# Kernel optimization log

Hardware: AMD Instinct MI355X
Metric: run time of the kernel (lower is better)

The kernel has to match this reference:

```python
import jax, jax.numpy as jnp
import numpy as np

EPS = 1e-06
K = 32


def setup_inputs() -> dict:
    key = jax.random.key(0)
    k1, k2, k3, k4, k5 = jax.random.split(key, 5)
    d_model, n_latents = 1024, 16384
    x = jax.random.normal(k1, (2, 2048, d_model), dtype=jnp.float32)
    b_pre = jax.random.normal(k2, (d_model,), dtype=jnp.float32) * 0.02
    W_enc = jax.random.normal(k3, (n_latents, d_model), dtype=jnp.float32) / np.sqrt(d_model)
    b_enc = jax.random.normal(k4, (n_latents,), dtype=jnp.float32) * 0.02
    W_dec = jax.random.normal(k5, (d_model, n_latents), dtype=jnp.float32)
    # mimic normalize_decoder_weights: unit norm along dim=1 (n_latents axis per row)
    W_dec = W_dec / jnp.linalg.norm(W_dec, axis=1, keepdims=True)
    return {"x": x, "b_pre": b_pre, "W_enc": W_enc, "b_enc": b_enc, "W_dec": W_dec}


def reference(x, b_pre, W_enc, b_enc, W_dec):
    B, S, D = x.shape
    # preprocess: center + normalize (torch .std is unbiased, ddof=1)
    mean = jnp.mean(x, axis=-1, keepdims=True)
    norm = jnp.std(x, axis=-1, keepdims=True, ddof=1) + EPS
    xn = ((x - mean) / norm).reshape(-1, D)          # [N, D]
    # encode
    h = (xn - b_pre) @ W_enc.T + b_enc               # [N, n_latents]
    # top-k + relu + scatter into sparse latent
    vals, idx = jax.lax.top_k(h, K)                  # [N, K]
    vals = jax.nn.relu(vals)
    rows = jnp.arange(h.shape[0])[:, None]
    h_sparse = jnp.zeros_like(h).at[rows, idx].set(vals)
    # decode (dense matmul over mostly-zero latents, as in the original)
    recon = h_sparse @ W_dec.T + b_pre               # [N, D]
    # postprocess: denormalize
    recon = recon.reshape(B, S, D) * norm + mean
    return recon
```

## Files before the change

kernel.cpp:

```cpp
#include <hip/hip_runtime.h>
#include <cstdint>
#include <cstddef>

typedef _Float16 half_t;
typedef _Float16 half4_t __attribute__((ext_vector_type(4)));
typedef _Float16 half8_t __attribute__((ext_vector_type(8)));
typedef unsigned short ushort8_t __attribute__((ext_vector_type(8)));
typedef float floatx4 __attribute__((ext_vector_type(4)));

#define NROWS 4096
#define DMODEL 1024
#define NLAT 16384
#define CAND_MAX 256

#define MBYTE (1ull << 20)
static const size_t oW0    = 0;
static const size_t oWdT   = 32 * MBYTE;
static const size_t oMeanD = 64 * MBYTE;
static const size_t oNormD = 64 * MBYTE + (64ull << 10);
static const size_t oCandC = 64 * MBYTE + (128ull << 10);
static const size_t oCandI = 65 * MBYTE;
static const size_t oBatch = 69 * MBYTE;

#define BATCH_ROW_BYTES 34816ull

__device__ __forceinline__ void gload16(const void* g, void* l) {
  __builtin_amdgcn_global_load_lds(
      (const __attribute__((address_space(1))) void*)g,
      (__attribute__((address_space(3))) void*)l, 16, 0, 0);
}

#define WSPLIT_B 2048
#define TRANS_B  4096
__global__ __launch_bounds__(256) void prepro_kernel(
    const float* __restrict__ x, const float* __restrict__ b_pre,
    const float* __restrict__ W_enc, const float* __restrict__ Wd,
    half_t* __restrict__ W0h, half_t* __restrict__ WdT,
    half_t* __restrict__ X0,
    double* __restrict__ meanD, double* __restrict__ normD, int r0) {
  int bid = blockIdx.x, tid = threadIdx.x;
  if (bid < WSPLIT_B) {
    size_t base = (size_t)bid * 2048 + tid;
    for (int it = 0; it < 8; ++it) {
      size_t i = base + (size_t)it * 256;
      float4 v = ((const float4*)W_enc)[i];
      half4_t h0;
      h0[0] = (half_t)(v.x * 1024.0f);
      h0[1] = (half_t)(v.y * 1024.0f);
      h0[2] = (half_t)(v.z * 1024.0f);
      h0[3] = (half_t)(v.w * 1024.0f);
      ((half4_t*)W0h)[i] = h0;
    }
    return;
  }
  if (bid < WSPLIT_B + TRANS_B) {
    __shared__ float tile[64][65];
    int t = bid - WSPLIT_B;
    int c0 = (t & 255) * 64;
    int r0t = (t >> 8) * 64;
    int tc = tid & 63, tg = tid >> 6;
    for (int i = 0; i < 16; ++i) {
      int rr = i * 4 + tg;
      tile[rr][tc] = Wd[(size_t)(r0t + rr) * NLAT + c0 + tc];
    }
    __syncthreads();
    for (int i = 0; i < 16; ++i) {
      int cc = i * 4 + tg;
      WdT[(size_t)(c0 + cc) * DMODEL + r0t + tc] = (half_t)tile[tc][cc];
    }
    return;
  }
  int rl = bid - WSPLIT_B - TRANS_B;
  int rg = r0 + rl;
  const float4* px = (const float4*)(x + (size_t)rg * DMODEL);
  float4 v = px[tid];
  double s  = (double)v.x + (double)v.y + (double)v.z + (double)v.w;
  double sq = (double)v.x * v.x + (double)v.y * v.y +
              (double)v.z * v.z + (double)v.w * v.w;
  for (int off = 32; off; off >>= 1) {
    s += __shfl_down(s, off);
    sq += __shfl_down(sq, off);
  }
  __shared__ double ss[4], ssq[4];
  __shared__ double sMean, sNorm;
  int wv = tid >> 6, ln = tid & 63;
  if (ln == 0) { ss[wv] = s; ssq[wv] = sq; }
  __syncthreads();
  if (tid == 0) {
    double S = ss[0] + ss[1] + ss[2] + ss[3];
    double Q = ssq[0] + ssq[1] + ssq[2] + ssq[3];
    double mean = S / (double)DMODEL;
    double var = (Q - (double)DMODEL * mean * mean) / (double)(DMODEL - 1);
    double nrm = sqrt(var) + 1e-6;
    sMean = mean; sNorm = nrm;
    meanD[rg] = mean; normD[rg] = nrm;
  }
  __syncthreads();
  float mean = (float)sMean, nrm = (float)sNorm;
  const float4* pb = (const float4*)b_pre;
  float4 bp = pb[tid];
  float c[4];
  c[0] = ((v.x - mean) / nrm - bp.x) * 1024.0f;
  c[1] = ((v.y - mean) / nrm - bp.y) * 1024.0f;
  c[2] = ((v.z - mean) / nrm - bp.z) * 1024.0f;
  c[3] = ((v.w - mean) / nrm - bp.w) * 1024.0f;
  half4_t h0;
  for (int i = 0; i < 4; ++i) h0[i] = (half_t)c[i];
  ((half4_t*)(X0 + (size_t)rl * DMODEL))[tid] = h0;
}

struct SmemAB { half_t A[2][256 * 64]; half_t B[2][256 * 64]; };
union SmemU { SmemAB ab; half_t c[256 * 256]; };

__global__ __launch_bounds__(512, 2) void gemm_enc(
    const half_t* __restrict__ X0, const half_t* __restrict__ W0,
    const float* __restrict__ b_enc, half_t* __restrict__ h, int mtiles) {
  __shared__ __align__(16) SmemU smem;
#define AS(b) (smem.ab.A[b])
#define BS(b) (smem.ab.B[b])
  int tid = threadIdx.x;
  int lane = tid & 63, wave = tid >> 6;
  int wm = wave >> 2, wn = wave & 3;

  int bid = blockIdx.x;
  int xcd = bid & 7, q = bid >> 3;
  int bn = xcd * 8 + (q & 7);
  int bm = q >> 3;
  (void)mtiles;

  const char* Ag = (const char*)(X0 + (size_t)bm * 256 * DMODEL);
  const char* Bg = (const char*)(W0 + (size_t)bn * 256 * DMODEL);

  int srcSwz = ((lane & 7) ^ (lane >> 3)) << 4;
  int rowBase = wave * 8 + (lane >> 3);
  int ldsWOff = wave * 1024;

#define STG_A(b, kt, pr) { int colB = ((kt) & 15) * 128 + srcSwz;             \
    gload16(Ag + (size_t)((pr) * 64 + rowBase) * 2048 + colB,                 \
            (char*)AS(b) + (pr) * 8192 + ldsWOff);                            \
    gload16(Ag + (size_t)(((pr) + 2) * 64 + rowBase) * 2048 + colB,           \
            (char*)AS(b) + ((pr) + 2) * 8192 + ldsWOff); }
#define STG_B(b, kt, pr) { int colB = ((kt) & 15) * 128 + srcSwz;             \
    gload16(Bg + (size_t)((pr) * 64 + rowBase) * 2048 + colB,                 \
            (char*)BS(b) + (pr) * 8192 + ldsWOff);                            \
    gload16(Bg + (size_t)(((pr) + 2) * 64 + rowBase) * 2048 + colB,           \
            (char*)BS(b) + ((pr) + 2) * 8192 + ldsWOff); }

  floatx4 acc[8][4] = {};

  STG_B(0, 0, 0); STG_B(0, 0, 1); STG_A(0, 0, 0); STG_A(0, 0, 1);
  STG_B(1, 1, 0); STG_B(1, 1, 1); STG_A(1, 1, 0);
  asm volatile("s_waitcnt vmcnt(6)" ::: "memory");
  __builtin_amdgcn_sched_barrier(0);
  __builtin_amdgcn_s_barrier();

  int laneQ = (lane & 15) * 128 + (lane >> 4) * 16;
  int sxor = (lane & 7) << 4;
  int aRow = wm * 128 * 128;
  int bRow = wn * 64 * 128;

  half8_t bfr[2][4], afA[4], afB[4];
  const char *Ab, *Bb;

#define LD_B(kk) _Pragma("unroll") for (int t = 0; t < 4; ++t)                \
    bfr[kk][t] = *(const half8_t*)(Bb + ((bRow + t * 2048 +                   \
                                          (kk) * 64 + laneQ) ^ sxor));
#define LD_AF(DST, mh, kk) _Pragma("unroll") for (int t = 0; t < 4; ++t)      \
    DST[t] = *(const half8_t*)(Ab + ((aRow + ((mh) * 4 + t) * 2048 +          \
                                      (kk) * 64 + laneQ) ^ sxor));
#define MM(mb, FR, kk) __builtin_amdgcn_s_setprio(1);                         \
    _Pragma("unroll") for (int mi = 0; mi < 4; ++mi)                          \
    _Pragma("unroll") for (int ni = 0; ni < 4; ++ni)                          \
      acc[(mb) + mi][ni] = __builtin_amdgcn_mfma_f32_16x16x32_f16(            \
          FR[mi], bfr[kk][ni], acc[(mb) + mi][ni], 0, 0, 0);                  \
    __builtin_amdgcn_s_setprio(0);
#define BAR() __builtin_amdgcn_s_barrier()
#define LGKM(n) { asm volatile("s_waitcnt lgkmcnt(" #n ")" ::: "memory");     \
    __builtin_amdgcn_sched_barrier(0); }
#define VM6() { asm volatile("s_waitcnt vmcnt(6)" ::: "memory");              \
    __builtin_amdgcn_sched_barrier(0); }
#define VM0() { asm volatile("s_waitcnt vmcnt(0)" ::: "memory");              \
    __builtin_amdgcn_sched_barrier(0); }

#pragma unroll 1
  for (int i = 0; i < 7; ++i) {
    int t0 = 2 * i;
    Ab = (const char*)AS(0); Bb = (const char*)BS(0);
    LD_B(0); LD_B(1); LD_AF(afA, 0, 0); LD_AF(afB, 1, 0);
    STG_A(1, t0 + 1, 1);
    BAR(); LGKM(4); MM(0, afA, 0); BAR();
    LD_AF(afA, 0, 1);
    STG_B(0, t0 + 2, 0);
    BAR(); LGKM(4); MM(4, afB, 0); BAR();
    LD_AF(afB, 1, 1);
    STG_B(0, t0 + 2, 1);
    BAR(); LGKM(4); MM(0, afA, 1); BAR();
    STG_A(0, t0 + 2, 0);
    BAR(); LGKM(0); MM(4, afB, 1); VM6(); BAR();
    Ab = (const char*)AS(1); Bb = (const char*)BS(1);
    LD_B(0); LD_B(1); LD_AF(afA, 0, 0); LD_AF(afB, 1, 0);
    STG_A(0, t0 + 2, 1);
    BAR(); LGKM(4); MM(0, afA, 0); BAR();
    LD_AF(afA, 0, 1);
    STG_B(1, t0 + 3, 0);
    BAR(); LGKM(4); MM(4, afB, 0); BAR();
    LD_AF(afB, 1, 1);
    STG_B(1, t0 + 3, 1);
    BAR(); LGKM(4); MM(0, afA, 1); BAR();
    STG_A(1, t0 + 3, 0);
    BAR(); LGKM(0); MM(4, afB, 1); VM6(); BAR();
  }
  {
    Ab = (const char*)AS(0); Bb = (const char*)BS(0);
    LD_B(0); LD_B(1); LD_AF(afA, 0, 0); LD_AF(afB, 1, 0);
    STG_A(1, 15, 1);
    BAR(); LGKM(4); MM(0, afA, 0); BAR();
    LD_AF(afA, 0, 1);
    BAR(); LGKM(4); MM(4, afB, 0); BAR();
    LD_AF(afB, 1, 1);
    BAR(); LGKM(4); MM(0, afA, 1); BAR();
    BAR(); LGKM(0); MM(4, afB, 1); VM0(); BAR();
    Ab = (const char*)AS(1); Bb = (const char*)BS(1);
    LD_B(0); LD_B(1); LD_AF(afA, 0, 0); LD_AF(afB, 1, 0);
    LGKM(4); MM(0, afA, 0);
    LD_AF(afA, 0, 1);
    LGKM(4); MM(4, afB, 0);
    LD_AF(afB, 1, 1);
    LGKM(4); MM(0, afA, 1);
    LGKM(0); MM(4, afB, 1);
  }
#undef STG_A
#undef STG_B
#undef LD_B
#undef LD_AF
#undef MM
#undef BAR
#undef LGKM
#undef VM6
#undef VM0

  __syncthreads();
  const float scale = 0x1p-20f;
  half_t* Cs = smem.c;
  {
    int lcBase = wn * 64 + (lane & 15);
    int lrBase = wm * 128 + (lane >> 4) * 4;
    float be[4];
#pragma unroll
    for (int ni = 0; ni < 4; ++ni) be[ni] = b_enc[bn * 256 + lcBase + ni * 16];
#pragma unroll
    for (int mi = 0; mi < 8; ++mi)
#pragma unroll
      for (int ni = 0; ni < 4; ++ni) {
        int lc = lcBase + ni * 16;
#pragma unroll
        for (int r = 0; r < 4; ++r) {
          int lr = lrBase + mi * 16 + r;
          half_t val = (half_t)(acc[mi][ni][r] * scale + be[ni]);
          int addr = lr * 512 + (((lc >> 3) ^ (lr & 15)) << 4) + ((lc & 7) << 1);
          *(half_t*)((char*)Cs + addr) = val;
        }
      }
  }
  __syncthreads();
  {
    int blk = lane & 31;
    int rsub = lane >> 5;
#pragma unroll
    for (int j = 0; j < 16; ++j) {
      int row = wave * 32 + j * 2 + rsub;
      int laddr = row * 512 + ((blk ^ (row & 15)) << 4);
      half8_t v = *(const half8_t*)((const char*)Cs + laddr);
      *(half8_t*)(h + (size_t)(bm * 256 + row) * NLAT + bn * 256 + blk * 8) = v;
    }
  }
#undef AS
#undef BS
}

__global__ __launch_bounds__(256) void cand_kernel(
    const half_t* __restrict__ h, int* __restrict__ candIdx,
    int* __restrict__ candCnt, int r0) {
  int rl = blockIdx.x, tid = threadIdx.x;
  int rg = r0 + rl;
  const ushort8_t* ph8 = (const ushort8_t*)(h + (size_t)rl * NLAT);

  __shared__ half_t hrow[NLAT];
  __shared__ float tmax[256];
  __shared__ float sThresh;
  __shared__ int cCount;

  if (tid == 0) cCount = 0;
  float m = -3.4e38f;
  for (int i = 0; i < 8; ++i) {
    ushort8_t v = ph8[tid + i * 256];
    ((ushort8_t*)hrow)[tid + i * 256] = v;
#pragma unroll
    for (int e = 0; e < 8; ++e) {
      float f = (float)__builtin_bit_cast(_Float16, (unsigned short)v[e]);
      m = fmaxf(m, f);
    }
  }
  tmax[tid] = m;
  __syncthreads();
  {
    int rank = 0;
    for (int o = 0; o < 256; ++o) {
      float vo = tmax[o];
      rank += (vo > m || (vo == m && o < tid)) ? 1 : 0;
    }
    if (rank == 31) sThresh = m - 0.02f;
  }
  __syncthreads();
  float thresh = sThresh;

  for (int i = 0; i < 8; ++i) {
    ushort8_t v = ((const ushort8_t*)hrow)[tid + i * 256];
#pragma unroll
    for (int e = 0; e < 8; ++e) {
      float f = (float)__builtin_bit_cast(_Float16, (unsigned short)v[e]);
      if (f >= thresh) {
        int slot = atomicAdd(&cCount, 1);
        if (slot < CAND_MAX) candIdx[(size_t)rg * CAND_MAX + slot] = (tid + i * 256) * 8 + e;
      }
    }
  }
  __syncthreads();
  if (tid == 0) candCnt[rg] = (cCount < CAND_MAX) ? cCount : CAND_MAX;
}

__global__ __launch_bounds__(256) void refine_sel_decode(
    const float* __restrict__ x, const float* __restrict__ b_pre,
    const float* __restrict__ W_enc, const float* __restrict__ b_enc,
    const double* __restrict__ meanD, const double* __restrict__ normD,
    const int* __restrict__ candIdx, const int* __restrict__ candCnt,
    const half_t* __restrict__ WdT, float* __restrict__ out, int r0) {
  int rg = r0 + blockIdx.x, tid = threadIdx.x;
  int wv = tid >> 6, ln = tid & 63;

  __shared__ int cI[CAND_MAX];
  __shared__ double cV[CAND_MAX];
  __shared__ float sVal[32];
  __shared__ int sIdx[32];

  double mean = meanD[rg], nrm = normD[rg];
  const float* px = x + (size_t)rg * DMODEL;
  double xr[16];
#pragma unroll
  for (int s = 0; s < 4; ++s) {
    float4 xv = *(const float4*)(px + s * 256 + 4 * ln);
    float4 bv = *(const float4*)(b_pre + s * 256 + 4 * ln);
    xr[s * 4 + 0] = ((double)xv.x - mean) / nrm - (double)bv.x;
    xr[s * 4 + 1] = ((double)xv.y - mean) / nrm - (double)bv.y;
    xr[s * 4 + 2] = ((double)xv.z - mean) / nrm - (double)bv.z;
    xr[s * 4 + 3] = ((double)xv.w - mean) / nrm - (double)bv.w;
  }
  int nc = candCnt[rg];
  for (int c = tid; c < nc; c += 256) cI[c] = candIdx[(size_t)rg * CAND_MAX + c];
  if (tid < 32) { sVal[tid] = 0.0f; sIdx[tid] = 0; }
  __syncthreads();

  for (int c0 = wv * 4; c0 < nc; c0 += 16) {
    const char* wp[4];
#pragma unroll
    for (int qq = 0; qq < 4; ++qq) {
      int c = c0 + qq;
      int j = cI[c < nc ? c : (nc - 1)];
      wp[qq] = (const char*)(W_enc + (size_t)j * DMODEL) + 16 * ln;
    }
    float4 w[4][4];
#pragma unroll
    for (int s = 0; s < 4; ++s)
#pragma unroll
      for (int qq = 0; qq < 4; ++qq)
        w[s][qq] = *(const float4*)(wp[qq] + s * 1024);
    double a0 = 0.0, a1 = 0.0, a2 = 0.0, a3 = 0.0;
#pragma unroll
    for (int s = 0; s < 4; ++s) {
      a0 += xr[s*4+0]*(double)w[s][0].x + xr[s*4+1]*(double)w[s][0].y +
            xr[s*4+2]*(double)w[s][0].z + xr[s*4+3]*(double)w[s][0].w;
      a1 += xr[s*4+0]*(double)w[s][1].x + xr[s*4+1]*(double)w[s][1].y +
            xr[s*4+2]*(double)w[s][1].z + xr[s*4+3]*(double)w[s][1].w;
      a2 += xr[s*4+0]*(double)w[s][2].x + xr[s*4+1]*(double)w[s][2].y +
            xr[s*4+2]*(double)w[s][2].z + xr[s*4+3]*(double)w[s][2].w;
      a3 += xr[s*4+0]*(double)w[s][3].x + xr[s*4+1]*(double)w[s][3].y +
            xr[s*4+2]*(double)w[s][3].z + xr[s*4+3]*(double)w[s][3].w;
    }
    double accq[4] = {a0, a1, a2, a3};
#pragma unroll
    for (int qq = 0; qq < 4; ++qq) {
      double s = accq[qq];
      for (int off = 32; off; off >>= 1) s += __shfl_down(s, off);
      int c = c0 + qq;
      if (ln == 0 && c < nc) cV[c] = s + (double)b_enc[cI[c]];
    }
  }
  __syncthreads();

  for (int c = tid; c < nc; c += 256) {
    double v = cV[c];
    int ix = cI[c];
    int rank = 0;
    for (int o = 0; o < nc; ++o) {
      double vo = cV[o];
      int io = cI[o];
      rank += (vo > v || (vo == v && io < ix)) ? 1 : 0;
    }
    if (rank < 32) {
      sIdx[rank] = ix;
      sVal[rank] = (float)(v > 0.0 ? v : 0.0);
    }
  }
  __syncthreads();

  int d0 = tid * 4;
  float4 accv = {0.f, 0.f, 0.f, 0.f};
#pragma unroll 8
  for (int k = 0; k < 32; ++k) {
    float vk = sVal[k];
    const half4_t wvv = *(const half4_t*)(WdT + (size_t)sIdx[k] * DMODEL + d0);
    accv.x += vk * (float)wvv[0]; accv.y += vk * (float)wvv[1];
    accv.z += vk * (float)wvv[2]; accv.w += vk * (float)wvv[3];
  }
  float4 bp = ((const float4*)b_pre)[tid];
  float nrmf = (float)nrm, mnf = (float)mean;
  float4 o;
  o.x = (accv.x + bp.x) * nrmf + mnf;
  o.y = (accv.y + bp.y) * nrmf + mnf;
  o.z = (accv.z + bp.z) * nrmf + mnf;
  o.w = (accv.w + bp.w) * nrmf + mnf;
  ((float4*)(out + (size_t)rg * DMODEL))[tid] = o;
}

extern "C" void kernel_launch(void* const* d_in, const int* in_sizes, int n_in,
                              void* d_out, int out_size, void* d_ws, size_t ws_size,
                              hipStream_t stream) {
  const float* x     = (const float*)d_in[0];
  const float* b_pre = (const float*)d_in[1];
  const float* W_enc = (const float*)d_in[2];
  const float* b_enc = (const float*)d_in[3];
  const float* W_dec = (const float*)d_in[4];
  float* out = (float*)d_out;
  char* ws = (char*)d_ws;

  int rowsB = NROWS;
  while (rowsB > 256) {
    size_t need = oBatch + (size_t)rowsB * BATCH_ROW_BYTES;
    if (need <= ws_size) break;
    rowsB >>= 1;
  }
  if (oBatch + (size_t)rowsB * BATCH_ROW_BYTES > ws_size) return;

  half_t* W0 = (half_t*)(ws + oW0);
  half_t* WdT = (half_t*)(ws + oWdT);
  double* meanD = (double*)(ws + oMeanD);
  double* normD = (double*)(ws + oNormD);
  int*   candCnt = (int*)(ws + oCandC);
  int*   candIdx = (int*)(ws + oCandI);
  half_t* X0b  = (half_t*)(ws + oBatch);
  half_t* hb   = X0b + (size_t)rowsB * DMODEL;

  for (int r0 = 0; r0 < NROWS; r0 += rowsB) {
    hipLaunchKernelGGL(prepro_kernel,
                       dim3(WSPLIT_B + TRANS_B + rowsB), dim3(256), 0, stream,
                       x, b_pre, W_enc, W_dec, W0, WdT, X0b, meanD, normD, r0);
    int mtiles = rowsB / 256;
    hipLaunchKernelGGL(gemm_enc, dim3(mtiles * 64), dim3(512), 0, stream,
                       X0b, W0, b_enc, hb, mtiles);
    hipLaunchKernelGGL(cand_kernel, dim3(rowsB), dim3(256), 0, stream,
                       hb, candIdx, candCnt, r0);
    hipLaunchKernelGGL(refine_sel_decode, dim3(rowsB), dim3(256), 0, stream,
                       x, b_pre, W_enc, b_enc, meanD, normD, candIdx, candCnt,
                       WdT, out, r0);
  }
}
```

Before: 348.6 us.

## Emit per-chunk maxima in GEMM epilogue and fuse candidate selection into decode

The encoder GEMM epilogue now computes a max over each 64-element chunk of h and writes it to a small per-row array. The separate candidate kernel, which re-read the full 16384-wide fp16 row, is removed. The decode kernel ranks the 256 chunk maxima to get a threshold and scans only the hot chunks of h to build candidates in shared memory. This cuts one full pass over h and one launch, at the cost of extra shuffles in the GEMM epilogue and a serial rank loop inside the decode kernel.

```diff
diff --git a/kernel.cpp b/kernel.cpp
--- a/kernel.cpp
+++ b/kernel.cpp
@@ -12,15 +12,15 @@
 #define DMODEL 1024
 #define NLAT 16384
 #define CAND_MAX 256
+#define NCHUNK 256
 
 #define MBYTE (1ull << 20)
 static const size_t oW0    = 0;
 static const size_t oWdT   = 32 * MBYTE;
 static const size_t oMeanD = 64 * MBYTE;
 static const size_t oNormD = 64 * MBYTE + (64ull << 10);
-static const size_t oCandC = 64 * MBYTE + (128ull << 10);
-static const size_t oCandI = 65 * MBYTE;
-static const size_t oBatch = 69 * MBYTE;
+static const size_t oCmax  = 65 * MBYTE;
+static const size_t oBatch = 68 * MBYTE;
 
 #define BATCH_ROW_BYTES 34816ull
 
@@ -114,7 +114,8 @@
 
 __global__ __launch_bounds__(512, 2) void gemm_enc(
     const half_t* __restrict__ X0, const half_t* __restrict__ W0,
-    const float* __restrict__ b_enc, half_t* __restrict__ h, int mtiles) {
+    const float* __restrict__ b_enc, half_t* __restrict__ h,
+    half_t* __restrict__ cmax, int mtiles) {
   __shared__ __align__(16) SmemU smem;
 #define AS(b) (smem.ab.A[b])
 #define BS(b) (smem.ab.B[b])
@@ -272,72 +273,35 @@
       int laddr = row * 512 + ((blk ^ (row & 15)) << 4);
       half8_t v = *(const half8_t*)((const char*)Cs + laddr);
       *(half8_t*)(h + (size_t)(bm * 256 + row) * NLAT + bn * 256 + blk * 8) = v;
+      float mx = (float)v[0];
+#pragma unroll
+      for (int e = 1; e < 8; ++e) mx = fmaxf(mx, (float)v[e]);
+      mx = fmaxf(mx, __shfl_xor(mx, 1));
+      mx = fmaxf(mx, __shfl_xor(mx, 2));
+      mx = fmaxf(mx, __shfl_xor(mx, 4));
+      if ((lane & 7) == 0)
+        cmax[(size_t)(bm * 256 + row) * NCHUNK + bn * 4 + (blk >> 3)] = (half_t)mx;
     }
   }
 #undef AS
 #undef BS
 }
 
-__global__ __launch_bounds__(256) void cand_kernel(
-    const half_t* __restrict__ h, int* __restrict__ candIdx,
-    int* __restrict__ candCnt, int r0) {
-  int rl = blockIdx.x, tid = threadIdx.x;
-  int rg = r0 + rl;
-  const ushort8_t* ph8 = (const ushort8_t*)(h + (size_t)rl * NLAT);
-
-  __shared__ half_t hrow[NLAT];
-  __shared__ float tmax[256];
-  __shared__ float sThresh;
-  __shared__ int cCount;
-
-  if (tid == 0) cCount = 0;
-  float m = -3.4e38f;
-  for (int i = 0; i < 8; ++i) {
-    ushort8_t v = ph8[tid + i * 256];
-    ((ushort8_t*)hrow)[tid + i * 256] = v;
-#pragma unroll
-    for (int e = 0; e < 8; ++e) {
-      float f = (float)__builtin_bit_cast(_Float16, (unsigned short)v[e]);
-      m = fmaxf(m, f);
-    }
-  }
-  tmax[tid] = m;
-  __syncthreads();
-  {
-    int rank = 0;
-    for (int o = 0; o < 256; ++o) {
-      float vo = tmax[o];
-      rank += (vo > m || (vo == m && o < tid)) ? 1 : 0;
-    }
-    if (rank == 31) sThresh = m - 0.02f;
-  }
-  __syncthreads();
-  float thresh = sThresh;
-
-  for (int i = 0; i < 8; ++i) {
-    ushort8_t v = ((const ushort8_t*)hrow)[tid + i * 256];
-#pragma unroll
-    for (int e = 0; e < 8; ++e) {
-      float f = (float)__builtin_bit_cast(_Float16, (unsigned short)v[e]);
-      if (f >= thresh) {
-        int slot = atomicAdd(&cCount, 1);
-        if (slot < CAND_MAX) candIdx[(size_t)rg * CAND_MAX + slot] = (tid + i * 256) * 8 + e;
-      }
-    }
-  }
-  __syncthreads();
-  if (tid == 0) candCnt[rg] = (cCount < CAND_MAX) ? cCount : CAND_MAX;
-}
-
-__global__ __launch_bounds__(256) void refine_sel_decode(
+__global__ __launch_bounds__(256) void postproc(
+    const half_t* __restrict__ h, const half_t* __restrict__ cmax,
     const float* __restrict__ x, const float* __restrict__ b_pre,
     const float* __restrict__ W_enc, const float* __restrict__ b_enc,
     const double* __restrict__ meanD, const double* __restrict__ normD,
-    const int* __restrict__ candIdx, const int* __restrict__ candCnt,
     const half_t* __restrict__ WdT, float* __restrict__ out, int r0) {
-  int rg = r0 + blockIdx.x, tid = threadIdx.x;
+  int rl = blockIdx.x, tid = threadIdx.x;
+  int rg = r0 + rl;
   int wv = tid >> 6, ln = tid & 63;
 
+  __shared__ float tmax[NCHUNK];
+  __shared__ float sThresh;
+  __shared__ int hotList[NCHUNK];
+  __shared__ int hotCnt;
+  __shared__ int cCount;
   __shared__ int cI[CAND_MAX];
   __shared__ double cV[CAND_MAX];
   __shared__ float sVal[32];
@@ -355,8 +319,43 @@
     xr[s * 4 + 2] = ((double)xv.z - mean) / nrm - (double)bv.z;
     xr[s * 4 + 3] = ((double)xv.w - mean) / nrm - (double)bv.w;
   }
-  int nc = candCnt[rg];
-  for (int c = tid; c < nc; c += 256) cI[c] = candIdx[(size_t)rg * CAND_MAX + c];
+
+  if (tid == 0) { cCount = 0; hotCnt = 0; }
+  float m = (float)cmax[(size_t)rl * NCHUNK + tid];
+  tmax[tid] = m;
+  __syncthreads();
+  {
+    int rank = 0;
+    for (int o = 0; o < NCHUNK; ++o) {
+      float vo = tmax[o];
+      rank += (vo > m || (vo == m && o < tid)) ? 1 : 0;
+    }
+    if (rank == 31) sThresh = m - 0.02f;
+  }
+  __syncthreads();
+  float thresh = sThresh;
+  if (m >= thresh) {
+    int slot = atomicAdd(&hotCnt, 1);
+    hotList[slot] = tid;
+  }
+  __syncthreads();
+  int nh = hotCnt;
+
+  const half_t* ph = h + (size_t)rl * NLAT;
+  for (int base = 0; base < nh; base += 4) {
+    int idx = base + wv;
+    if (idx < nh) {
+      int ch = hotList[idx];
+      int j = ch * 64 + ln;
+      float f = (float)ph[j];
+      if (f >= thresh) {
+        int slot = atomicAdd(&cCount, 1);
+        if (slot < CAND_MAX) cI[slot] = j;
+      }
+    }
+  }
+  __syncthreads();
+  int nc = (cCount < CAND_MAX) ? cCount : CAND_MAX;
   if (tid < 32) { sVal[tid] = 0.0f; sIdx[tid] = 0; }
   __syncthreads();
 
@@ -455,8 +454,7 @@
   half_t* WdT = (half_t*)(ws + oWdT);
   double* meanD = (double*)(ws + oMeanD);
   double* normD = (double*)(ws + oNormD);
-  int*   candCnt = (int*)(ws + oCandC);
-  int*   candIdx = (int*)(ws + oCandI);
+  half_t* cmaxA = (half_t*)(ws + oCmax);
   half_t* X0b  = (half_t*)(ws + oBatch);
   half_t* hb   = X0b + (size_t)rowsB * DMODEL;
 
@@ -466,11 +464,9 @@
                        x, b_pre, W_enc, W_dec, W0, WdT, X0b, meanD, normD, r0);
     int mtiles = rowsB / 256;
     hipLaunchKernelGGL(gemm_enc, dim3(mtiles * 64), dim3(512), 0, stream,
-                       X0b, W0, b_enc, hb, mtiles);
-    hipLaunchKernelGGL(cand_kernel, dim3(rowsB), dim3(256), 0, stream,
-                       hb, candIdx, candCnt, r0);
-    hipLaunchKernelGGL(refine_sel_decode, dim3(rowsB), dim3(256), 0, stream,
-                       x, b_pre, W_enc, b_enc, meanD, normD, candIdx, candCnt,
-                       WdT, out, r0);
+                       X0b, W0, b_enc, hb, cmaxA, mtiles);
+    hipLaunchKernelGGL(postproc, dim3(rowsB), dim3(256), 0, stream,
+                       hb, cmaxA, x, b_pre, W_enc, b_enc, meanD, normD, WdT,
+                       out, r0);
   }
 }
```

After: 329.1 us. 5.6% less time.
